# Optimization experiments

Measured on AMD Instinct MI355X. Metric: run time of the kernel, lower is better.

The kernel has to match this reference:

```python
import jax, jax.numpy as jnp
import numpy as np

BETA = 0.5
TAU_L = 0.1
TAU_H = 0.1
TOP_K = 2


def setup_inputs() -> dict:
    key = jax.random.key(0)
    ks = jax.random.split(key, 6)
    B, S, H, F, E, NH = 1, 2048, 1024, 3584, 8, 16
    hidden_states = jax.random.normal(ks[0], (B, S, H), dtype=jnp.float32)
    self_attn_weights = jax.random.uniform(ks[1], (B, NH, S, S), dtype=jnp.float32)
    gate_w = jax.random.normal(ks[2], (E, H), dtype=jnp.float32) * 0.02
    w1 = jax.random.normal(ks[3], (E, F, H), dtype=jnp.float32) * 0.02
    w2 = jax.random.normal(ks[4], (E, H, F), dtype=jnp.float32) * 0.02
    w3 = jax.random.normal(ks[5], (E, F, H), dtype=jnp.float32) * 0.02
    return {"hidden_states": hidden_states, "self_attn_weights": self_attn_weights,
            "gate_w": gate_w, "w1": w1, "w2": w2, "w3": w3}


def reference(hidden_states, self_attn_weights, gate_w, w1, w2, w3):
    B, S, H = hidden_states.shape
    E = gate_w.shape[0]
    x = hidden_states.reshape(-1, H)          # [T, H], T = B*S
    T = x.shape[0]

    router_logits = x @ gate_w.T              # [T, E]
    rw_full = jax.nn.softmax(router_logits.astype(jnp.float32), axis=-1)
    rw, sel = jax.lax.top_k(rw_full, TOP_K)   # [T, 2]

    # --- dynamic pruning branch (loss_index < block_range) ---
    mask_top1 = rw[:, 1] < BETA * rw[:, 0]
    new_routing = jnp.ones_like(rw)
    new_routing = new_routing.at[:, 1].set(jnp.where(mask_top1, 0.0, 1.0))

    # sequence_length > 1: attention-based token pruning (assumes B == 1)
    mean_tensor = jnp.mean(jnp.squeeze(self_attn_weights), axis=0)  # [S, S]
    column = mean_tensor.shape[1]
    real_number = jnp.arange(column, 0, -1, dtype=jnp.float32)
    attention_scores = jnp.sum(mean_tensor, axis=1) / real_number   # [S]
    l1_norm = jnp.sum(jnp.abs(x), axis=1)                           # [T]
    attention_scores = attention_scores * l1_norm

    n_low = int(TAU_L * T)
    n_high = int(TAU_H * T)
    _, low_idx = jax.lax.top_k(-attention_scores, n_low)   # smallest
    _, high_idx = jax.lax.top_k(attention_scores, n_high)  # largest
    mask_all = jnp.zeros((T,), dtype=bool).at[low_idx].set(True)
    keep_all = jnp.zeros((T,), dtype=bool).at[high_idx].set(True)
    new_routing = jnp.where(mask_all[:, None], 0.0, new_routing)
    new_routing = jnp.where(keep_all[:, None], 1.0, new_routing)

    rw = rw * new_routing
    denom = jnp.sum(rw, axis=-1, keepdims=True)
    rw = rw / jnp.where(denom > 0, denom, 1.0)  # fully-masked tokens -> 0 output
    rw = rw.astype(x.dtype)

    # combine weights per (token, expert); dispatch mask == new_routing
    cw = jnp.sum(rw[:, :, None] * jax.nn.one_hot(sel, E, dtype=rw.dtype), axis=1)  # [T, E]

    # dense reference for the gather-expert-scatter loop (SwiGLU experts)
    h = jnp.einsum('th,efh->tef', x, w1)      # [T, E, F]
    g = jnp.einsum('th,efh->tef', x, w3)
    a = jax.nn.silu(h) * g
    y = jnp.einsum('tef,ehf->teh', a, w2)     # [T, E, H]
    out = jnp.einsum('te,teh->th', cw, y)     # [T, H]

    return out.reshape(B, S, H), router_logits
```

## Files before the change

### kernel.cpp

```cpp
#include <hip/hip_runtime.h>
#include <hip/hip_bf16.h>
#include <math.h>

#define NTOK 2048
#define HDIM 1024
#define NEXP 8
#define FDIM 3584
#define NHEADS 16
#define NLOW 204
#define NHIGH 204
#define BK 64
#define KSPLIT 4
#define KCH (FDIM / KSPLIT)

typedef __bf16 bf16x8 __attribute__((ext_vector_type(8)));
typedef float f32x4 __attribute__((ext_vector_type(4)));

__device__ __forceinline__ void gload16(__hip_bfloat16* lds, const __hip_bfloat16* g)
{
    __builtin_amdgcn_global_load_lds(
        (const __attribute__((address_space(1))) unsigned int*)g,
        (__attribute__((address_space(3))) unsigned int*)lds, 16, 0, 0);
}

__global__ __launch_bounds__(256) void k_xbf16(
    const float* __restrict__ x, __hip_bfloat16* __restrict__ xb)
{
    int i = (blockIdx.x * 256 + threadIdx.x) * 8;
    float4 a = *(const float4*)(x + i);
    float4 b = *(const float4*)(x + i + 4);
    bf16x8 v;
    v[0] = (__bf16)a.x; v[1] = (__bf16)a.y; v[2] = (__bf16)a.z; v[3] = (__bf16)a.w;
    v[4] = (__bf16)b.x; v[5] = (__bf16)b.y; v[6] = (__bf16)b.z; v[7] = (__bf16)b.w;
    *(bf16x8*)(xb + i) = v;
}

__global__ __launch_bounds__(256) void k_w16(
    const float* __restrict__ src, __hip_bfloat16* __restrict__ dst)
{
    size_t i = ((size_t)blockIdx.x * 256 + threadIdx.x) * 8;
    float4 a = *(const float4*)(src + i);
    float4 b = *(const float4*)(src + i + 4);
    bf16x8 v;
    v[0] = (__bf16)a.x; v[1] = (__bf16)a.y; v[2] = (__bf16)a.z; v[3] = (__bf16)a.w;
    v[4] = (__bf16)b.x; v[5] = (__bf16)b.y; v[6] = (__bf16)b.z; v[7] = (__bf16)b.w;
    *(bf16x8*)(dst + i) = v;
}

__global__ __launch_bounds__(256) void k_router(
    const float* __restrict__ x, const float* __restrict__ gw,
    float* __restrict__ logits, float* __restrict__ l1,
    int* __restrict__ sel0, int* __restrict__ sel1,
    float* __restrict__ rw0, float* __restrict__ rw1)
{
    __shared__ float sgw[NEXP * HDIM];
    int tid = threadIdx.x;
    for (int i = tid; i < NEXP * HDIM; i += 256) sgw[i] = gw[i];
    __syncthreads();
    int wv = tid >> 6, lane = tid & 63;
    int t = blockIdx.x * 4 + wv;
    const float* xr = x + (size_t)t * HDIM;
    float acc[NEXP];
#pragma unroll
    for (int e = 0; e < NEXP; ++e) acc[e] = 0.f;
    float al1 = 0.f;
    for (int h = lane; h < HDIM; h += 64) {
        float xv = xr[h];
        al1 += fabsf(xv);
#pragma unroll
        for (int e = 0; e < NEXP; ++e) acc[e] += xv * sgw[e * HDIM + h];
    }
#pragma unroll
    for (int off = 32; off > 0; off >>= 1) {
#pragma unroll
        for (int e = 0; e < NEXP; ++e) acc[e] += __shfl_xor(acc[e], off);
        al1 += __shfl_xor(al1, off);
    }
    if (lane < NEXP) logits[t * NEXP + lane] = acc[lane];
    if (lane == 0) {
        l1[t] = al1;
        float m = acc[0];
#pragma unroll
        for (int e = 1; e < NEXP; ++e) m = fmaxf(m, acc[e]);
        float p[NEXP], s = 0.f;
#pragma unroll
        for (int e = 0; e < NEXP; ++e) { p[e] = expf(acc[e] - m); s += p[e]; }
        float inv = 1.f / s;
        float b0 = -1.f, b1 = -1.f; int i0 = 0, i1 = 0;
#pragma unroll
        for (int e = 0; e < NEXP; ++e) {
            float r = p[e] * inv;
            if (r > b0) { b1 = b0; i1 = i0; b0 = r; i0 = e; }
            else if (r > b1) { b1 = r; i1 = e; }
        }
        sel0[t] = i0; sel1[t] = i1; rw0[t] = b0; rw1[t] = b1;
    }
}

__global__ __launch_bounds__(256) void k_attn(
    const float* __restrict__ attn, const float* __restrict__ l1,
    float* __restrict__ scores)
{
    int i = blockIdx.x, tid = threadIdx.x;
    float acc = 0.f;
    for (int h = 0; h < NHEADS; ++h) {
        const float4* p = (const float4*)(attn + ((size_t)h * NTOK + i) * NTOK);
        for (int j = tid; j < NTOK / 4; j += 256) {
            float4 v = p[j];
            acc += v.x + v.y + v.z + v.w;
        }
    }
    __shared__ float red[256];
    red[tid] = acc; __syncthreads();
    for (int s = 128; s > 0; s >>= 1) {
        if (tid < s) red[tid] += red[tid + s];
        __syncthreads();
    }
    if (tid == 0) scores[i] = red[0] / (16.f * (float)(NTOK - i)) * l1[i];
}

__global__ __launch_bounds__(256) void k_rank(
    const float* __restrict__ scores, const float* __restrict__ rw0,
    const float* __restrict__ rw1, float* __restrict__ w0f, float* __restrict__ w1f)
{
    __shared__ float s[NTOK];
    int tid = threadIdx.x;
    for (int i = tid; i < NTOK; i += 256) s[i] = scores[i];
    __syncthreads();
    int t = blockIdx.x * 256 + tid;
    float st = s[t];
    int cl = 0, ch = 0;
    for (int j = 0; j < NTOK; ++j) {
        float sj = s[j];
        int tie = (sj == st) && (j < t);
        cl += (sj < st) || tie;
        ch += (sj > st) || tie;
    }
    bool in_low = cl < NLOW, keep = ch < NHIGH;
    float a = rw0[t], b = rw1[t];
    float n0 = 1.f, n1 = (b < 0.5f * a) ? 0.f : 1.f;
    if (in_low) { n0 = 0.f; n1 = 0.f; }
    if (keep)   { n0 = 1.f; n1 = 1.f; }
    a *= n0; b *= n1;
    float d = a + b;
    if (d > 0.f) { a /= d; b /= d; }
    w0f[t] = a; w1f[t] = b;
}

__global__ __launch_bounds__(512) void k_build(
    const int* __restrict__ sel0, const int* __restrict__ sel1,
    const float* __restrict__ w0f, const float* __restrict__ w1f,
    int* __restrict__ tok, float* __restrict__ wgt,
    int* __restrict__ counts, int* __restrict__ offs)
{
    int tid = threadIdx.x;
    int e = tid >> 6, lane = tid & 63;
    unsigned long long below = (1ull << lane) - 1ull;
    int base = 0;
    for (int r = 0; r < NTOK / 64; ++r) {
        int t = r * 64 + lane;
        bool f0 = (sel0[t] == e) && (w0f[t] > 0.f);
        unsigned long long m0 = __ballot(f0);
        if (f0) {
            int pos = base + __popcll(m0 & below);
            tok[e * NTOK + pos] = t; wgt[e * NTOK + pos] = w0f[t];
        }
        base += __popcll(m0);
        bool f1 = (sel1[t] == e) && (w1f[t] > 0.f);
        unsigned long long m1 = __ballot(f1);
        if (f1) {
            int pos = base + __popcll(m1 & below);
            tok[e * NTOK + pos] = t; wgt[e * NTOK + pos] = w1f[t];
        }
        base += __popcll(m1);
    }
    if (lane == 0) counts[e] = base;
    __syncthreads();
    if (tid == 0) {
        int o = 0;
        for (int i = 0; i < NEXP; ++i) { offs[i] = o; o += counts[i]; }
    }
}

__global__ __launch_bounds__(256) void k_zero(float4* __restrict__ out)
{
    out[blockIdx.x * 256 + threadIdx.x] = make_float4(0.f, 0.f, 0.f, 0.f);
}

__global__ __launch_bounds__(256, 3) void k_ffn1(
    const __hip_bfloat16* __restrict__ xb, const __hip_bfloat16* __restrict__ wb1,
    const __hip_bfloat16* __restrict__ wb3,
    const int* __restrict__ tok, const float* __restrict__ wgt,
    const int* __restrict__ counts, const int* __restrict__ offs,
    __hip_bfloat16* __restrict__ act)
{
    int e = blockIdx.z;
    int cnt = counts[e];
    int m0 = blockIdx.y * 128;
    if (m0 >= cnt) return;
    int f0 = blockIdx.x * 64;
    int tid = threadIdx.x;
    __shared__ __align__(16) __hip_bfloat16 sX[128 * BK];
    __shared__ __align__(16) __hip_bfloat16 sW1[64 * BK];
    __shared__ __align__(16) __hip_bfloat16 sW3[64 * BK];
    __shared__ int sTok[128];
    __shared__ float sWgt[128];
    if (tid < 128) {
        int row = m0 + tid;
        int rr = (row < cnt) ? row : (cnt - 1);
        sTok[tid] = tok[e * NTOK + rr];
        sWgt[tid] = (row < cnt) ? wgt[e * NTOK + row] : 0.f;
    }
    __syncthreads();

    int wv = tid >> 6, lane = tid & 63;
    int lr = lane >> 3;
    int sw8 = (((lane & 7) ^ lr) << 3);

    const __hip_bfloat16* gx[4];
    __hip_bfloat16* lx[4];
#pragma unroll
    for (int j = 0; j < 4; ++j) {
        int c = 4 * wv + j;
        gx[j] = xb + (size_t)sTok[8 * c + lr] * HDIM + sw8;
        lx[j] = sX + c * 512;
    }
    const __hip_bfloat16* gw1[2]; const __hip_bfloat16* gw3[2];
    __hip_bfloat16* lw1[2]; __hip_bfloat16* lw3[2];
#pragma unroll
    for (int j = 0; j < 2; ++j) {
        int c = 2 * wv + j;
        gw1[j] = wb1 + ((size_t)e * FDIM + f0 + 8 * c + lr) * HDIM + sw8;
        gw3[j] = wb3 + ((size_t)e * FDIM + f0 + 8 * c + lr) * HDIM + sw8;
        lw1[j] = sW1 + c * 512;
        lw3[j] = sW3 + c * 512;
    }

    int colx = lane & 15;
    int swz = (colx & 7) << 4;
    int kb0 = (lane >> 4) * 16;
    f32x4 acc1[2][4] = {}, acc3[2][4] = {};

    for (int k0 = 0; k0 < HDIM; k0 += BK) {
#pragma unroll
        for (int j = 0; j < 4; ++j) gload16(lx[j], gx[j] + k0);
#pragma unroll
        for (int j = 0; j < 2; ++j) {
            gload16(lw1[j], gw1[j] + k0);
            gload16(lw3[j], gw3[j] + k0);
        }
        __syncthreads();
#pragma unroll
        for (int ks = 0; ks < 2; ++ks) {
            int off = ((kb0 + ks * 64) ^ swz) >> 1;
            bf16x8 a_[2];
#pragma unroll
            for (int m = 0; m < 2; ++m) {
                int row = 32 * wv + m * 16 + colx;
                a_[m] = *(const bf16x8*)&sX[(row << 6) + off];
            }
#pragma unroll
            for (int f = 0; f < 4; ++f) {
                int row = f * 16 + colx;
                bf16x8 b1 = *(const bf16x8*)&sW1[(row << 6) + off];
                bf16x8 b3 = *(const bf16x8*)&sW3[(row << 6) + off];
#pragma unroll
                for (int m = 0; m < 2; ++m) {
                    acc1[m][f] = __builtin_amdgcn_mfma_f32_16x16x32_bf16(a_[m], b1, acc1[m][f], 0, 0, 0);
                    acc3[m][f] = __builtin_amdgcn_mfma_f32_16x16x32_bf16(a_[m], b3, acc3[m][f], 0, 0, 0);
                }
            }
        }
        __syncthreads();
    }
    int soff = offs[e];
    int lane4 = (lane >> 4) * 4;
#pragma unroll
    for (int m = 0; m < 2; ++m) {
        int rbase = 32 * wv + m * 16 + lane4;
#pragma unroll
        for (int q = 0; q < 4; ++q) {
            int rloc = rbase + q;
            if (m0 + rloc < cnt) {
                float wgtv = sWgt[rloc];
#pragma unroll
                for (int f = 0; f < 4; ++f) {
                    float hv = acc1[m][f][q], gv = acc3[m][f][q];
                    float av = hv / (1.f + expf(-hv)) * gv * wgtv;
                    act[(size_t)(soff + m0 + rloc) * FDIM + f0 + f * 16 + colx] =
                        (__hip_bfloat16)av;
                }
            }
        }
    }
}

__global__ __launch_bounds__(256, 4) void k_ffn2(
    const __hip_bfloat16* __restrict__ act, const __hip_bfloat16* __restrict__ wb2,
    const int* __restrict__ tok, const int* __restrict__ counts,
    const int* __restrict__ offs, float* __restrict__ out)
{
    int z = blockIdx.z;
    int e = z >> 2;
    int kbase = (z & 3) * KCH;
    int cnt = counts[e];
    int m0 = blockIdx.y * 128;
    if (m0 >= cnt) return;
    int h0 = blockIdx.x * 64;
    int tid = threadIdx.x;
    __shared__ __align__(16) __hip_bfloat16 sA[128 * BK];
    __shared__ __align__(16) __hip_bfloat16 sB[64 * BK];
    __shared__ int sTok[128];
    if (tid < 128) {
        int row = m0 + tid;
        sTok[tid] = (row < cnt) ? tok[e * NTOK + row] : 0;
    }
    __syncthreads();
    int soff = offs[e];
    int wv = tid >> 6, lane = tid & 63;
    int lr = lane >> 3;
    int sw8 = (((lane & 7) ^ lr) << 3);

    const __hip_bfloat16* ga[4];
    __hip_bfloat16* la[4];
#pragma unroll
    for (int j = 0; j < 4; ++j) {
        int c = 4 * wv + j;
        int trow = 8 * c + lr;
        int arow = (m0 + trow < cnt) ? (m0 + trow) : (cnt - 1);
        ga[j] = act + (size_t)(soff + arow) * FDIM + kbase + sw8;
        la[j] = sA + c * 512;
    }
    const __hip_bfloat16* gb[2];
    __hip_bfloat16* lb[2];
#pragma unroll
    for (int j = 0; j < 2; ++j) {
        int c = 2 * wv + j;
        gb[j] = wb2 + ((size_t)e * HDIM + h0 + 8 * c + lr) * FDIM + kbase + sw8;
        lb[j] = sB + c * 512;
    }

    int colx = lane & 15;
    int swz = (colx & 7) << 4;
    int kb0 = (lane >> 4) * 16;
    f32x4 acc[2][4] = {};

    for (int k0 = 0; k0 < KCH; k0 += BK) {
#pragma unroll
        for (int j = 0; j < 4; ++j) gload16(la[j], ga[j] + k0);
#pragma unroll
        for (int j = 0; j < 2; ++j) gload16(lb[j], gb[j] + k0);
        __syncthreads();
#pragma unroll
        for (int ks = 0; ks < 2; ++ks) {
            int off = ((kb0 + ks * 64) ^ swz) >> 1;
            bf16x8 a_[2];
#pragma unroll
            for (int m = 0; m < 2; ++m) {
                int row = 32 * wv + m * 16 + colx;
                a_[m] = *(const bf16x8*)&sA[(row << 6) + off];
            }
#pragma unroll
            for (int f = 0; f < 4; ++f) {
                int row = f * 16 + colx;
                bf16x8 b = *(const bf16x8*)&sB[(row << 6) + off];
#pragma unroll
                for (int m = 0; m < 2; ++m)
                    acc[m][f] = __builtin_amdgcn_mfma_f32_16x16x32_bf16(a_[m], b, acc[m][f], 0, 0, 0);
            }
        }
        __syncthreads();
    }
    int lane4 = (lane >> 4) * 4;
#pragma unroll
    for (int m = 0; m < 2; ++m) {
        int rbase = 32 * wv + m * 16 + lane4;
#pragma unroll
        for (int q = 0; q < 4; ++q) {
            int rloc = rbase + q;
            if (m0 + rloc < cnt) {
                int t = sTok[rloc];
#pragma unroll
                for (int f = 0; f < 4; ++f)
                    atomicAdd(&out[(size_t)t * HDIM + h0 + f * 16 + colx], acc[m][f][q]);
            }
        }
    }
}

extern "C" void kernel_launch(void* const* d_in, const int* in_sizes, int n_in,
                              void* d_out, int out_size, void* d_ws, size_t ws_size,
                              hipStream_t stream)
{
    const float* x    = (const float*)d_in[0];
    const float* attn = (const float*)d_in[1];
    const float* gw   = (const float*)d_in[2];
    const float* w1   = (const float*)d_in[3];
    const float* w2   = (const float*)d_in[4];
    const float* w3   = (const float*)d_in[5];
    float* out = (float*)d_out;
    float* logits = out + (size_t)NTOK * HDIM;

    char* ws = (char*)d_ws;
    float* l1     = (float*)(ws + 0);
    float* scores = (float*)(ws + 8192);
    int*   sel0   = (int*)(ws + 16384);
    int*   sel1   = (int*)(ws + 24576);
    float* rw0    = (float*)(ws + 32768);
    float* rw1    = (float*)(ws + 40960);
    float* w0f    = (float*)(ws + 49152);
    float* w1f    = (float*)(ws + 57344);
    int*   counts = (int*)(ws + 65536);
    int*   offs   = (int*)(ws + 65600);
    int*   tok    = (int*)(ws + 73728);
    float* wgt    = (float*)(ws + 143360);
    __hip_bfloat16* act = (__hip_bfloat16*)(ws + 1048576);
    __hip_bfloat16* xb  = (__hip_bfloat16*)(ws + 33554432);
    __hip_bfloat16* wb1 = (__hip_bfloat16*)(ws + 67108864);
    __hip_bfloat16* wb3 = (__hip_bfloat16*)(ws + 134217728);
    __hip_bfloat16* wb2 = (__hip_bfloat16*)(ws + 201326592);

    const int NW = NEXP * FDIM * HDIM;

    k_xbf16<<<NTOK * HDIM / (256 * 8), 256, 0, stream>>>(x, xb);
    k_w16<<<NW / (256 * 8), 256, 0, stream>>>(w1, wb1);
    k_w16<<<NW / (256 * 8), 256, 0, stream>>>(w3, wb3);
    k_w16<<<NW / (256 * 8), 256, 0, stream>>>(w2, wb2);
    k_router<<<NTOK / 4, 256, 0, stream>>>(x, gw, logits, l1, sel0, sel1, rw0, rw1);
    k_attn<<<NTOK, 256, 0, stream>>>(attn, l1, scores);
    k_rank<<<NTOK / 256, 256, 0, stream>>>(scores, rw0, rw1, w0f, w1f);
    k_build<<<1, 512, 0, stream>>>(sel0, sel1, w0f, w1f, tok, wgt, counts, offs);
    k_zero<<<NTOK, 256, 0, stream>>>((float4*)out);
    k_ffn1<<<dim3(FDIM / 64, NTOK / 128, NEXP), 256, 0, stream>>>(
        xb, wb1, wb3, tok, wgt, counts, offs, act);
    k_ffn2<<<dim3(HDIM / 64, NTOK / 128, NEXP * KSPLIT), 256, 0, stream>>>(
        act, wb2, tok, counts, offs, out);
}
```

Measured before the change: 413.5 us.

## Enlarge FFN GEMM tiles, fuse prep kernels, overlap w2 conversion with ffn1

```diff
diff --git a/kernel.cpp b/kernel.cpp
--- a/kernel.cpp
+++ b/kernel.cpp
@@ -23,28 +23,43 @@
         (__attribute__((address_space(3))) unsigned int*)lds, 16, 0, 0);
 }
 
-__global__ __launch_bounds__(256) void k_xbf16(
-    const float* __restrict__ x, __hip_bfloat16* __restrict__ xb)
-{
-    int i = (blockIdx.x * 256 + threadIdx.x) * 8;
-    float4 a = *(const float4*)(x + i);
-    float4 b = *(const float4*)(x + i + 4);
+__device__ __forceinline__ void cvt8(const float* __restrict__ s,
+                                     __hip_bfloat16* __restrict__ d)
+{
+    float4 a = *(const float4*)s;
+    float4 b = *(const float4*)(s + 4);
     bf16x8 v;
     v[0] = (__bf16)a.x; v[1] = (__bf16)a.y; v[2] = (__bf16)a.z; v[3] = (__bf16)a.w;
     v[4] = (__bf16)b.x; v[5] = (__bf16)b.y; v[6] = (__bf16)b.z; v[7] = (__bf16)b.w;
-    *(bf16x8*)(xb + i) = v;
-}
-
-__global__ __launch_bounds__(256) void k_w16(
-    const float* __restrict__ src, __hip_bfloat16* __restrict__ dst)
-{
-    size_t i = ((size_t)blockIdx.x * 256 + threadIdx.x) * 8;
-    float4 a = *(const float4*)(src + i);
-    float4 b = *(const float4*)(src + i + 4);
-    bf16x8 v;
-    v[0] = (__bf16)a.x; v[1] = (__bf16)a.y; v[2] = (__bf16)a.z; v[3] = (__bf16)a.w;
-    v[4] = (__bf16)b.x; v[5] = (__bf16)b.y; v[6] = (__bf16)b.z; v[7] = (__bf16)b.w;
-    *(bf16x8*)(dst + i) = v;
+    *(bf16x8*)d = v;
+}
+
+#define NZ   (NTOK * HDIM / 4)
+#define NX   (NTOK * HDIM / 8)
+#define NWT  (NEXP * FDIM * HDIM / 8)
+__global__ __launch_bounds__(256) void k_prep(
+    const float* __restrict__ x, const float* __restrict__ w1,
+    const float* __restrict__ w3, float4* __restrict__ outz,
+    __hip_bfloat16* __restrict__ xb, __hip_bfloat16* __restrict__ wb1,
+    __hip_bfloat16* __restrict__ wb3)
+{
+    size_t gid = (size_t)blockIdx.x * 256 + threadIdx.x;
+    size_t stride = (size_t)gridDim.x * 256;
+    size_t total = (size_t)NZ + NX + 2 * (size_t)NWT;
+    for (size_t i = gid; i < total; i += stride) {
+        if (i < NZ) {
+            outz[i] = make_float4(0.f, 0.f, 0.f, 0.f);
+        } else if (i < (size_t)NZ + NX) {
+            size_t j = (i - NZ) * 8;
+            cvt8(x + j, xb + j);
+        } else if (i < (size_t)NZ + NX + NWT) {
+            size_t j = (i - NZ - NX) * 8;
+            cvt8(w1 + j, wb1 + j);
+        } else {
+            size_t j = (i - NZ - NX - NWT) * 8;
+            cvt8(w3 + j, wb3 + j);
+        }
+    }
 }
 
 __global__ __launch_bounds__(256) void k_router(
@@ -182,27 +197,30 @@
     }
 }
 
-__global__ __launch_bounds__(256) void k_zero(float4* __restrict__ out)
-{
-    out[blockIdx.x * 256 + threadIdx.x] = make_float4(0.f, 0.f, 0.f, 0.f);
-}
-
-__global__ __launch_bounds__(256, 3) void k_ffn1(
+__global__ __launch_bounds__(256, 2) void k_ffn1(
     const __hip_bfloat16* __restrict__ xb, const __hip_bfloat16* __restrict__ wb1,
     const __hip_bfloat16* __restrict__ wb3,
+    const float* __restrict__ w2, __hip_bfloat16* __restrict__ wb2,
     const int* __restrict__ tok, const float* __restrict__ wgt,
     const int* __restrict__ counts, const int* __restrict__ offs,
     __hip_bfloat16* __restrict__ act)
 {
+    int tid = threadIdx.x;
+    if (blockIdx.z == NEXP) {
+        size_t gid = ((size_t)(blockIdx.y * gridDim.x + blockIdx.x) * 256 + tid);
+        size_t stride = (size_t)gridDim.x * gridDim.y * 256;
+        for (size_t i = gid; i < (size_t)NWT; i += stride)
+            cvt8(w2 + i * 8, wb2 + i * 8);
+        return;
+    }
     int e = blockIdx.z;
     int cnt = counts[e];
     int m0 = blockIdx.y * 128;
     if (m0 >= cnt) return;
-    int f0 = blockIdx.x * 64;
-    int tid = threadIdx.x;
+    int f0 = blockIdx.x * 128;
     __shared__ __align__(16) __hip_bfloat16 sX[128 * BK];
-    __shared__ __align__(16) __hip_bfloat16 sW1[64 * BK];
-    __shared__ __align__(16) __hip_bfloat16 sW3[64 * BK];
+    __shared__ __align__(16) __hip_bfloat16 sW1[128 * BK];
+    __shared__ __align__(16) __hip_bfloat16 sW3[128 * BK];
     __shared__ int sTok[128];
     __shared__ float sWgt[128];
     if (tid < 128) {
@@ -217,35 +235,29 @@
     int lr = lane >> 3;
     int sw8 = (((lane & 7) ^ lr) << 3);
 
-    const __hip_bfloat16* gx[4];
-    __hip_bfloat16* lx[4];
+    const __hip_bfloat16* gx[4]; const __hip_bfloat16* gw1[4]; const __hip_bfloat16* gw3[4];
+    __hip_bfloat16 *lx[4], *lw1[4], *lw3[4];
 #pragma unroll
     for (int j = 0; j < 4; ++j) {
         int c = 4 * wv + j;
-        gx[j] = xb + (size_t)sTok[8 * c + lr] * HDIM + sw8;
-        lx[j] = sX + c * 512;
-    }
-    const __hip_bfloat16* gw1[2]; const __hip_bfloat16* gw3[2];
-    __hip_bfloat16* lw1[2]; __hip_bfloat16* lw3[2];
-#pragma unroll
-    for (int j = 0; j < 2; ++j) {
-        int c = 2 * wv + j;
+        gx[j]  = xb  + (size_t)sTok[8 * c + lr] * HDIM + sw8;
+        lx[j]  = sX  + c * 512;
         gw1[j] = wb1 + ((size_t)e * FDIM + f0 + 8 * c + lr) * HDIM + sw8;
+        lw1[j] = sW1 + c * 512;
         gw3[j] = wb3 + ((size_t)e * FDIM + f0 + 8 * c + lr) * HDIM + sw8;
-        lw1[j] = sW1 + c * 512;
         lw3[j] = sW3 + c * 512;
     }
 
     int colx = lane & 15;
     int swz = (colx & 7) << 4;
     int kb0 = (lane >> 4) * 16;
-    f32x4 acc1[2][4] = {}, acc3[2][4] = {};
+    int wm = (wv >> 1) * 64, wf = (wv & 1) * 64;
+    f32x4 acc1[4][4] = {}, acc3[4][4] = {};
 
     for (int k0 = 0; k0 < HDIM; k0 += BK) {
 #pragma unroll
-        for (int j = 0; j < 4; ++j) gload16(lx[j], gx[j] + k0);
-#pragma unroll
-        for (int j = 0; j < 2; ++j) {
+        for (int j = 0; j < 4; ++j) {
+            gload16(lx[j],  gx[j]  + k0);
             gload16(lw1[j], gw1[j] + k0);
             gload16(lw3[j], gw3[j] + k0);
         }
@@ -253,19 +265,17 @@
 #pragma unroll
         for (int ks = 0; ks < 2; ++ks) {
             int off = ((kb0 + ks * 64) ^ swz) >> 1;
-            bf16x8 a_[2];
-#pragma unroll
-            for (int m = 0; m < 2; ++m) {
-                int row = 32 * wv + m * 16 + colx;
-                a_[m] = *(const bf16x8*)&sX[(row << 6) + off];
-            }
+            bf16x8 a_[4];
+#pragma unroll
+            for (int m = 0; m < 4; ++m)
+                a_[m] = *(const bf16x8*)&sX[((wm + m * 16 + colx) << 6) + off];
 #pragma unroll
             for (int f = 0; f < 4; ++f) {
-                int row = f * 16 + colx;
+                int row = wf + f * 16 + colx;
                 bf16x8 b1 = *(const bf16x8*)&sW1[(row << 6) + off];
                 bf16x8 b3 = *(const bf16x8*)&sW3[(row << 6) + off];
 #pragma unroll
-                for (int m = 0; m < 2; ++m) {
+                for (int m = 0; m < 4; ++m) {
                     acc1[m][f] = __builtin_amdgcn_mfma_f32_16x16x32_bf16(a_[m], b1, acc1[m][f], 0, 0, 0);
                     acc3[m][f] = __builtin_amdgcn_mfma_f32_16x16x32_bf16(a_[m], b3, acc3[m][f], 0, 0, 0);
                 }
@@ -276,8 +286,8 @@
     int soff = offs[e];
     int lane4 = (lane >> 4) * 4;
 #pragma unroll
-    for (int m = 0; m < 2; ++m) {
-        int rbase = 32 * wv + m * 16 + lane4;
+    for (int m = 0; m < 4; ++m) {
+        int rbase = wm + m * 16 + lane4;
 #pragma unroll
         for (int q = 0; q < 4; ++q) {
             int rloc = rbase + q;
@@ -287,7 +297,7 @@
                 for (int f = 0; f < 4; ++f) {
                     float hv = acc1[m][f][q], gv = acc3[m][f][q];
                     float av = hv / (1.f + expf(-hv)) * gv * wgtv;
-                    act[(size_t)(soff + m0 + rloc) * FDIM + f0 + f * 16 + colx] =
+                    act[(size_t)(soff + m0 + rloc) * FDIM + f0 + wf + f * 16 + colx] =
                         (__hip_bfloat16)av;
                 }
             }
@@ -295,7 +305,7 @@
     }
 }
 
-__global__ __launch_bounds__(256, 4) void k_ffn2(
+__global__ __launch_bounds__(256, 3) void k_ffn2(
     const __hip_bfloat16* __restrict__ act, const __hip_bfloat16* __restrict__ wb2,
     const int* __restrict__ tok, const int* __restrict__ counts,
     const int* __restrict__ offs, float* __restrict__ out)
@@ -306,10 +316,10 @@
     int cnt = counts[e];
     int m0 = blockIdx.y * 128;
     if (m0 >= cnt) return;
-    int h0 = blockIdx.x * 64;
+    int h0 = blockIdx.x * 128;
     int tid = threadIdx.x;
     __shared__ __align__(16) __hip_bfloat16 sA[128 * BK];
-    __shared__ __align__(16) __hip_bfloat16 sB[64 * BK];
+    __shared__ __align__(16) __hip_bfloat16 sB[128 * BK];
     __shared__ int sTok[128];
     if (tid < 128) {
         int row = m0 + tid;
@@ -321,8 +331,8 @@
     int lr = lane >> 3;
     int sw8 = (((lane & 7) ^ lr) << 3);
 
-    const __hip_bfloat16* ga[4];
-    __hip_bfloat16* la[4];
+    const __hip_bfloat16* ga[4]; const __hip_bfloat16* gb[4];
+    __hip_bfloat16 *la[4], *lb[4];
 #pragma unroll
     for (int j = 0; j < 4; ++j) {
         int c = 4 * wv + j;
@@ -330,42 +340,35 @@
         int arow = (m0 + trow < cnt) ? (m0 + trow) : (cnt - 1);
         ga[j] = act + (size_t)(soff + arow) * FDIM + kbase + sw8;
         la[j] = sA + c * 512;
-    }
-    const __hip_bfloat16* gb[2];
-    __hip_bfloat16* lb[2];
-#pragma unroll
-    for (int j = 0; j < 2; ++j) {
-        int c = 2 * wv + j;
-        gb[j] = wb2 + ((size_t)e * HDIM + h0 + 8 * c + lr) * FDIM + kbase + sw8;
+        gb[j] = wb2 + ((size_t)e * HDIM + h0 + trow) * FDIM + kbase + sw8;
         lb[j] = sB + c * 512;
     }
 
     int colx = lane & 15;
     int swz = (colx & 7) << 4;
     int kb0 = (lane >> 4) * 16;
-    f32x4 acc[2][4] = {};
+    int wm = (wv >> 1) * 64, wh = (wv & 1) * 64;
+    f32x4 acc[4][4] = {};
 
     for (int k0 = 0; k0 < KCH; k0 += BK) {
 #pragma unroll
-        for (int j = 0; j < 4; ++j) gload16(la[j], ga[j] + k0);
-#pragma unroll
-        for (int j = 0; j < 2; ++j) gload16(lb[j], gb[j] + k0);
+        for (int j = 0; j < 4; ++j) {
+            gload16(la[j], ga[j] + k0);
+            gload16(lb[j], gb[j] + k0);
+        }
         __syncthreads();
 #pragma unroll
         for (int ks = 0; ks < 2; ++ks) {
             int off = ((kb0 + ks * 64) ^ swz) >> 1;
-            bf16x8 a_[2];
-#pragma unroll
-            for (int m = 0; m < 2; ++m) {
-                int row = 32 * wv + m * 16 + colx;
-                a_[m] = *(const bf16x8*)&sA[(row << 6) + off];
-            }
+            bf16x8 a_[4];
+#pragma unroll
+            for (int m = 0; m < 4; ++m)
+                a_[m] = *(const bf16x8*)&sA[((wm + m * 16 + colx) << 6) + off];
 #pragma unroll
             for (int f = 0; f < 4; ++f) {
-                int row = f * 16 + colx;
-                bf16x8 b = *(const bf16x8*)&sB[(row << 6) + off];
-#pragma unroll
-                for (int m = 0; m < 2; ++m)
+                bf16x8 b = *(const bf16x8*)&sB[((wh + f * 16 + colx) << 6) + off];
+#pragma unroll
+                for (int m = 0; m < 4; ++m)
                     acc[m][f] = __builtin_amdgcn_mfma_f32_16x16x32_bf16(a_[m], b, acc[m][f], 0, 0, 0);
             }
         }
@@ -373,8 +376,8 @@
     }
     int lane4 = (lane >> 4) * 4;
 #pragma unroll
-    for (int m = 0; m < 2; ++m) {
-        int rbase = 32 * wv + m * 16 + lane4;
+    for (int m = 0; m < 4; ++m) {
+        int rbase = wm + m * 16 + lane4;
 #pragma unroll
         for (int q = 0; q < 4; ++q) {
             int rloc = rbase + q;
@@ -382,7 +385,7 @@
                 int t = sTok[rloc];
 #pragma unroll
                 for (int f = 0; f < 4; ++f)
-                    atomicAdd(&out[(size_t)t * HDIM + h0 + f * 16 + colx], acc[m][f][q]);
+                    atomicAdd(&out[(size_t)t * HDIM + h0 + wh + f * 16 + colx], acc[m][f][q]);
             }
         }
     }
@@ -420,19 +423,13 @@
     __hip_bfloat16* wb3 = (__hip_bfloat16*)(ws + 134217728);
     __hip_bfloat16* wb2 = (__hip_bfloat16*)(ws + 201326592);
 
-    const int NW = NEXP * FDIM * HDIM;
-
-    k_xbf16<<<NTOK * HDIM / (256 * 8), 256, 0, stream>>>(x, xb);
-    k_w16<<<NW / (256 * 8), 256, 0, stream>>>(w1, wb1);
-    k_w16<<<NW / (256 * 8), 256, 0, stream>>>(w3, wb3);
-    k_w16<<<NW / (256 * 8), 256, 0, stream>>>(w2, wb2);
+    k_prep<<<4096, 256, 0, stream>>>(x, w1, w3, (float4*)out, xb, wb1, wb3);
     k_router<<<NTOK / 4, 256, 0, stream>>>(x, gw, logits, l1, sel0, sel1, rw0, rw1);
     k_attn<<<NTOK, 256, 0, stream>>>(attn, l1, scores);
     k_rank<<<NTOK / 256, 256, 0, stream>>>(scores, rw0, rw1, w0f, w1f);
     k_build<<<1, 512, 0, stream>>>(sel0, sel1, w0f, w1f, tok, wgt, counts, offs);
-    k_zero<<<NTOK, 256, 0, stream>>>((float4*)out);
-    k_ffn1<<<dim3(FDIM / 64, NTOK / 128, NEXP), 256, 0, stream>>>(
-        xb, wb1, wb3, tok, wgt, counts, offs, act);
-    k_ffn2<<<dim3(HDIM / 64, NTOK / 128, NEXP * KSPLIT), 256, 0, stream>>>(
+    k_ffn1<<<dim3(FDIM / 128, NTOK / 128, NEXP + 1), 256, 0, stream>>>(
+        xb, wb1, wb3, w2, wb2, tok, wgt, counts, offs, act);
+    k_ffn2<<<dim3(HDIM / 128, NTOK / 128, NEXP * KSPLIT), 256, 0, stream>>>(
         act, wb2, tok, counts, offs, out);
 }
```

Measured after the change: 422.7 us. +2.2%, slower.

## Fuse conversion kernels and overlap w2 conversion with first expert GEMM

Applied to the files above, without the earlier changes.

```diff
diff --git a/kernel.cpp b/kernel.cpp
--- a/kernel.cpp
+++ b/kernel.cpp
@@ -23,28 +23,43 @@
         (__attribute__((address_space(3))) unsigned int*)lds, 16, 0, 0);
 }
 
-__global__ __launch_bounds__(256) void k_xbf16(
-    const float* __restrict__ x, __hip_bfloat16* __restrict__ xb)
-{
-    int i = (blockIdx.x * 256 + threadIdx.x) * 8;
-    float4 a = *(const float4*)(x + i);
-    float4 b = *(const float4*)(x + i + 4);
+__device__ __forceinline__ void cvt8(const float* __restrict__ s,
+                                     __hip_bfloat16* __restrict__ d)
+{
+    float4 a = *(const float4*)s;
+    float4 b = *(const float4*)(s + 4);
     bf16x8 v;
     v[0] = (__bf16)a.x; v[1] = (__bf16)a.y; v[2] = (__bf16)a.z; v[3] = (__bf16)a.w;
     v[4] = (__bf16)b.x; v[5] = (__bf16)b.y; v[6] = (__bf16)b.z; v[7] = (__bf16)b.w;
-    *(bf16x8*)(xb + i) = v;
-}
-
-__global__ __launch_bounds__(256) void k_w16(
-    const float* __restrict__ src, __hip_bfloat16* __restrict__ dst)
-{
-    size_t i = ((size_t)blockIdx.x * 256 + threadIdx.x) * 8;
-    float4 a = *(const float4*)(src + i);
-    float4 b = *(const float4*)(src + i + 4);
-    bf16x8 v;
-    v[0] = (__bf16)a.x; v[1] = (__bf16)a.y; v[2] = (__bf16)a.z; v[3] = (__bf16)a.w;
-    v[4] = (__bf16)b.x; v[5] = (__bf16)b.y; v[6] = (__bf16)b.z; v[7] = (__bf16)b.w;
-    *(bf16x8*)(dst + i) = v;
+    *(bf16x8*)d = v;
+}
+
+#define NZ   (NTOK * HDIM / 4)
+#define NX   (NTOK * HDIM / 8)
+#define NWT  (NEXP * FDIM * HDIM / 8)
+__global__ __launch_bounds__(256) void k_prep(
+    const float* __restrict__ x, const float* __restrict__ w1,
+    const float* __restrict__ w3, float4* __restrict__ outz,
+    __hip_bfloat16* __restrict__ xb, __hip_bfloat16* __restrict__ wb1,
+    __hip_bfloat16* __restrict__ wb3)
+{
+    size_t gid = (size_t)blockIdx.x * 256 + threadIdx.x;
+    size_t stride = (size_t)gridDim.x * 256;
+    size_t total = (size_t)NZ + NX + 2 * (size_t)NWT;
+    for (size_t i = gid; i < total; i += stride) {
+        if (i < NZ) {
+            outz[i] = make_float4(0.f, 0.f, 0.f, 0.f);
+        } else if (i < (size_t)NZ + NX) {
+            size_t j = (i - NZ) * 8;
+            cvt8(x + j, xb + j);
+        } else if (i < (size_t)NZ + NX + NWT) {
+            size_t j = (i - NZ - NX) * 8;
+            cvt8(w1 + j, wb1 + j);
+        } else {
+            size_t j = (i - NZ - NX - NWT) * 8;
+            cvt8(w3 + j, wb3 + j);
+        }
+    }
 }
 
 __global__ __launch_bounds__(256) void k_router(
@@ -182,24 +197,27 @@
     }
 }
 
-__global__ __launch_bounds__(256) void k_zero(float4* __restrict__ out)
-{
-    out[blockIdx.x * 256 + threadIdx.x] = make_float4(0.f, 0.f, 0.f, 0.f);
-}
-
 __global__ __launch_bounds__(256, 3) void k_ffn1(
     const __hip_bfloat16* __restrict__ xb, const __hip_bfloat16* __restrict__ wb1,
     const __hip_bfloat16* __restrict__ wb3,
+    const float* __restrict__ w2, __hip_bfloat16* __restrict__ wb2,
     const int* __restrict__ tok, const float* __restrict__ wgt,
     const int* __restrict__ counts, const int* __restrict__ offs,
     __hip_bfloat16* __restrict__ act)
 {
-    int e = blockIdx.z;
+    int tid = threadIdx.x;
+    if (blockIdx.z == 0) {
+        size_t gid = ((size_t)(blockIdx.y * gridDim.x + blockIdx.x) * 256 + tid);
+        size_t stride = (size_t)gridDim.x * gridDim.y * 256;
+        for (size_t i = gid; i < (size_t)NWT; i += stride)
+            cvt8(w2 + i * 8, wb2 + i * 8);
+        return;
+    }
+    int e = blockIdx.z - 1;
     int cnt = counts[e];
     int m0 = blockIdx.y * 128;
     if (m0 >= cnt) return;
     int f0 = blockIdx.x * 64;
-    int tid = threadIdx.x;
     __shared__ __align__(16) __hip_bfloat16 sX[128 * BK];
     __shared__ __align__(16) __hip_bfloat16 sW1[64 * BK];
     __shared__ __align__(16) __hip_bfloat16 sW3[64 * BK];
@@ -420,19 +438,13 @@
     __hip_bfloat16* wb3 = (__hip_bfloat16*)(ws + 134217728);
     __hip_bfloat16* wb2 = (__hip_bfloat16*)(ws + 201326592);
 
-    const int NW = NEXP * FDIM * HDIM;
-
-    k_xbf16<<<NTOK * HDIM / (256 * 8), 256, 0, stream>>>(x, xb);
-    k_w16<<<NW / (256 * 8), 256, 0, stream>>>(w1, wb1);
-    k_w16<<<NW / (256 * 8), 256, 0, stream>>>(w3, wb3);
-    k_w16<<<NW / (256 * 8), 256, 0, stream>>>(w2, wb2);
+    k_prep<<<4096, 256, 0, stream>>>(x, w1, w3, (float4*)out, xb, wb1, wb3);
     k_router<<<NTOK / 4, 256, 0, stream>>>(x, gw, logits, l1, sel0, sel1, rw0, rw1);
     k_attn<<<NTOK, 256, 0, stream>>>(attn, l1, scores);
     k_rank<<<NTOK / 256, 256, 0, stream>>>(scores, rw0, rw1, w0f, w1f);
     k_build<<<1, 512, 0, stream>>>(sel0, sel1, w0f, w1f, tok, wgt, counts, offs);
-    k_zero<<<NTOK, 256, 0, stream>>>((float4*)out);
-    k_ffn1<<<dim3(FDIM / 64, NTOK / 128, NEXP), 256, 0, stream>>>(
-        xb, wb1, wb3, tok, wgt, counts, offs, act);
+    k_ffn1<<<dim3(FDIM / 64, NTOK / 128, NEXP + 1), 256, 0, stream>>>(
+        xb, wb1, wb3, w2, wb2, tok, wgt, counts, offs, act);
     k_ffn2<<<dim3(HDIM / 64, NTOK / 128, NEXP * KSPLIT), 256, 0, stream>>>(
         act, wb2, tok, counts, offs, out);
 }
```

Measured after the change: 407.2 us (median of 2 runs). No clear change (-1.5%).
